# Optimization experiments

Hardware: AMD Instinct MI355X
Metric: run time of the kernel (lower is better)

The kernel has to match this reference:

```python
import jax, jax.numpy as jnp
import numpy as np

LN_EPS = 1e-5
NUM_EXPERTS = 8

def setup_inputs() -> dict:
    key = jax.random.key(0)
    ks = jax.random.split(key, 8)
    B, S, D = 8, 2048, 2048
    R = D // 4  # reduced_dim = 512
    E = NUM_EXPERTS
    scale1 = 1.0 / np.sqrt(D)
    scale2 = 1.0 / np.sqrt(R)
    return {
        "hidden_states": jax.random.normal(ks[0], (B, S, D), dtype=jnp.float32),
        "ln_gamma": jnp.ones((D,), dtype=jnp.float32),
        "ln_beta": jnp.zeros((D,), dtype=jnp.float32),
        "w1": jax.random.uniform(ks[1], (D, R), minval=-scale1, maxval=scale1, dtype=jnp.float32),
        "b1": jax.random.uniform(ks[2], (R,), minval=-scale1, maxval=scale1, dtype=jnp.float32),
        "w2": jax.random.uniform(ks[3], (R, R), minval=-scale2, maxval=scale2, dtype=jnp.float32),
        "b2": jax.random.uniform(ks[4], (R,), minval=-scale2, maxval=scale2, dtype=jnp.float32),
        "wr": jax.random.uniform(ks[5], (R, E), minval=-scale2, maxval=scale2, dtype=jnp.float32),
        "br": jax.random.uniform(ks[6], (E,), minval=-scale2, maxval=scale2, dtype=jnp.float32),
    }

def reference(hidden_states, ln_gamma, ln_beta, w1, b1, w2, b2, wr, br):
    # LayerNorm over last dim (eps matches torch default 1e-5)
    mu = jnp.mean(hidden_states, axis=-1, keepdims=True)
    var = jnp.mean(jnp.square(hidden_states - mu), axis=-1, keepdims=True)
    x = (hidden_states - mu) * jax.lax.rsqrt(var + LN_EPS) * ln_gamma + ln_beta
    # Linear -> GELU (exact, torch default) -> Linear
    h = jax.nn.gelu(jnp.einsum('bsd,dr->bsr', x, w1) + b1, approximate=False)
    t = jnp.einsum('bsr,rq->bsq', h, w2) + b2  # [B,S,R]
    batch_reduced = jnp.sum(t, axis=1)          # [B,R]
    router_logits = batch_reduced @ wr + br     # [B,E]
    # top-1 expert per batch element; one-hot targets via scatter
    expert_indices = jnp.argmax(router_logits, axis=-1)                 # [B]
    targets = jax.nn.one_hot(expert_indices, router_logits.shape[-1],
                             dtype=router_logits.dtype)                 # [B,E]
    # BCE-with-logits, mean over all elements: log(1+e^x) - x*t
    aux_loss = jnp.mean(jnp.logaddexp(0.0, router_logits) - router_logits * targets)
    # mode over batch of top-1 indices (torch .mode returns smallest on ties;
    # argmax of bincount picks the first/smallest max index -> matches)
    counts = jnp.sum(targets, axis=0)
    next_idx = jnp.argmax(counts)
    return aux_loss, next_idx
```

## Files before the change

### kernel.cpp

```cpp
#include <hip/hip_runtime.h>
#include <math.h>

#define D_DIM 2048
#define R_DIM 512
#define E_NUM 8
#define B_NUM 8
#define S_NUM 2048
#define M_DIM 16384
#define LN_EPS 1e-5f

typedef __attribute__((ext_vector_type(8))) short bf16x8;
typedef __attribute__((ext_vector_type(4))) float f32x4;

__device__ __forceinline__ unsigned short f2bf(float f) {
    unsigned u = __float_as_uint(f);
    return (unsigned short)((u + 0x7FFFu + ((u >> 16) & 1u)) >> 16);
}

__device__ __forceinline__ void gload_lds16(const void* g, void* l) {
    __builtin_amdgcn_global_load_lds(
        (const __attribute__((address_space(1))) void*)g,
        (__attribute__((address_space(3))) void*)l, 16, 0, 0);
}

__global__ __launch_bounds__(256) void prep_kernel(float* __restrict__ x,
                                                   const float* __restrict__ gamma,
                                                   const float* __restrict__ beta,
                                                   const float* __restrict__ w1,
                                                   unsigned short* __restrict__ wt,
                                                   float* __restrict__ zbuf) {
    const int t = threadIdx.x;
    if (blockIdx.x < M_DIM) {
        __shared__ float sred[8];
        float* row = x + (size_t)blockIdx.x * D_DIM;
        const float4 v0  = ((const float4*)row)[t];
        const float4 v1  = ((const float4*)row)[t + 256];
        const float4 g0  = ((const float4*)gamma)[t];
        const float4 g1  = ((const float4*)gamma)[t + 256];
        const float4 be0 = ((const float4*)beta)[t];
        const float4 be1 = ((const float4*)beta)[t + 256];

        float s  = v0.x + v0.y + v0.z + v0.w + v1.x + v1.y + v1.z + v1.w;
        float sq = v0.x*v0.x + v0.y*v0.y + v0.z*v0.z + v0.w*v0.w
                 + v1.x*v1.x + v1.y*v1.y + v1.z*v1.z + v1.w*v1.w;
#pragma unroll
        for (int off = 32; off > 0; off >>= 1) {
            s  += __shfl_down(s, off);
            sq += __shfl_down(sq, off);
        }
        if ((t & 63) == 0) { sred[(t >> 6) * 2] = s; sred[(t >> 6) * 2 + 1] = sq; }
        __syncthreads();
        s  = sred[0] + sred[2] + sred[4] + sred[6];
        sq = sred[1] + sred[3] + sred[5] + sred[7];
        const float mu  = s * (1.f / D_DIM);
        const float var = sq * (1.f / D_DIM) - mu * mu;
        const float rs  = rsqrtf(var + LN_EPS);

        ushort4 h0, h1;
        h0.x = f2bf(fmaf((v0.x - mu) * rs, g0.x, be0.x));
        h0.y = f2bf(fmaf((v0.y - mu) * rs, g0.y, be0.y));
        h0.z = f2bf(fmaf((v0.z - mu) * rs, g0.z, be0.z));
        h0.w = f2bf(fmaf((v0.w - mu) * rs, g0.w, be0.w));
        h1.x = f2bf(fmaf((v1.x - mu) * rs, g1.x, be1.x));
        h1.y = f2bf(fmaf((v1.y - mu) * rs, g1.y, be1.y));
        h1.z = f2bf(fmaf((v1.z - mu) * rs, g1.z, be1.z));
        h1.w = f2bf(fmaf((v1.w - mu) * rs, g1.w, be1.w));

        ushort4* rowu = (ushort4*)row;
        rowu[t]       = h0;
        rowu[t + 256] = h1;
    } else if (blockIdx.x < M_DIM + 1024) {
        const int tid = (blockIdx.x - M_DIM) * 256 + t;
        const int n  = tid >> 9;
        const int k4 = tid & 511;
        ushort4 h;
        h.x = f2bf(w1[(size_t)(k4 * 4 + 0) * R_DIM + n]);
        h.y = f2bf(w1[(size_t)(k4 * 4 + 1) * R_DIM + n]);
        h.z = f2bf(w1[(size_t)(k4 * 4 + 2) * R_DIM + n]);
        h.w = f2bf(w1[(size_t)(k4 * 4 + 3) * R_DIM + n]);
        ((ushort4*)wt)[(size_t)n * 512 + k4] = h;
    } else {
        zbuf[(blockIdx.x - M_DIM - 1024) * 256 + t] = 0.f;
    }
}

#define BM 128
#define BN 128
#define BK 64

__global__ __launch_bounds__(256, 2) void gemm_kernel(
    const unsigned short* __restrict__ xs,
    const unsigned short* __restrict__ wt,
    const float* __restrict__ b1,
    float* __restrict__ hsum) {
    __shared__ __align__(16) unsigned short lds[2 * 8192];

    const int t = threadIdx.x, lane = t & 63, wid = t >> 6;
    const int xcd = blockIdx.x & 7, i0 = blockIdx.x >> 3;
    const int n0 = (xcd >> 1) * BN;
    const int m0 = ((xcd & 1) * 64 + i0) * BM;
    const int mw = wid >> 1, nw = wid & 1;
    const int fr = lane & 15, kg = lane >> 4, fr7 = lane & 7;

    f32x4 acc[4][4];
#pragma unroll
    for (int i = 0; i < 4; ++i)
#pragma unroll
        for (int j = 0; j < 4; ++j) acc[i][j] = (f32x4){0.f, 0.f, 0.f, 0.f};

    int srow[4], sgo[4], ldso[4];
#pragma unroll
    for (int ii = 0; ii < 4; ++ii) {
        const int idx = wid * 4 + ii;
        const int o = (idx << 10) + (lane << 4);
        const int r = o >> 7, sl = (o >> 4) & 7;
        srow[ii] = r;
        sgo[ii]  = ((sl ^ (r & 7)) << 4);
        ldso[ii] = (idx << 10);
    }

    int aoff[4], boff[4];
#pragma unroll
    for (int f = 0; f < 4; ++f) {
        aoff[f] = (mw * 64 + f * 16 + fr) * 128;
        boff[f] = (nw * 64 + f * 16 + fr) * 128;
    }
    const char* ldsb = (const char*)lds;

    for (int k0b = 0; k0b < D_DIM * 2; k0b += BK * 2) {
        __syncthreads();
#pragma unroll
        for (int ii = 0; ii < 4; ++ii) {
            const char* a = (const char*)xs + (size_t)(m0 + srow[ii]) * 8192 + k0b + sgo[ii];
            const char* b = (const char*)wt + (size_t)(n0 + srow[ii]) * 4096 + k0b + sgo[ii];
            gload_lds16(a, (char*)lds +     0 + ldso[ii]);
            gload_lds16(b, (char*)lds + 16384 + ldso[ii]);
        }
        __syncthreads();
#pragma unroll
        for (int kk = 0; kk < 2; ++kk) {
            const int sw = ((kk * 4 + kg) ^ fr7) << 4;
            bf16x8 ah[4], bh[4];
#pragma unroll
            for (int f = 0; f < 4; ++f) {
                ah[f] = *(const bf16x8*)(ldsb +     0 + aoff[f] + sw);
                bh[f] = *(const bf16x8*)(ldsb + 16384 + boff[f] + sw);
            }
#pragma unroll
            for (int i = 0; i < 4; ++i)
#pragma unroll
                for (int j = 0; j < 4; ++j)
                    acc[i][j] = __builtin_amdgcn_mfma_f32_16x16x32_bf16(ah[i], bh[j], acc[i][j], 0, 0, 0);
        }
    }

    __syncthreads();
    float* red = (float*)lds;
    float pn[4];
#pragma unroll
    for (int j = 0; j < 4; ++j) pn[j] = 0.f;
#pragma unroll
    for (int j = 0; j < 4; ++j) {
        const float bb = b1[n0 + nw * 64 + j * 16 + fr];
#pragma unroll
        for (int i = 0; i < 4; ++i)
#pragma unroll
            for (int r = 0; r < 4; ++r) {
                const float y = acc[i][j][r] + bb;
                pn[j] += 0.5f * y * (1.f + erff(y * 0.70710678118654752f));
            }
    }
#pragma unroll
    for (int j = 0; j < 4; ++j)
        red[(wid * 4 + kg) * 64 + j * 16 + fr] = pn[j];
    __syncthreads();
    if (t < 128) {
        const int nw2 = t >> 6, cl = t & 63;
        float s2 = 0.f;
#pragma unroll
        for (int mw2 = 0; mw2 < 2; ++mw2)
#pragma unroll
            for (int g = 0; g < 4; ++g)
                s2 += red[((mw2 * 2 + nw2) * 4 + g) * 64 + cl];
        atomicAdd(&hsum[(m0 >> 11) * R_DIM + n0 + t], s2);
    }
}

__global__ void router1_kernel(const float* __restrict__ hsum,
                               const float* __restrict__ w2,
                               const float* __restrict__ b2,
                               float* __restrict__ brd) {
    const int q  = blockIdx.x * 64 + threadIdx.x;
    const int r0 = blockIdx.y * 64;
    float acc[8] = {0, 0, 0, 0, 0, 0, 0, 0};
    for (int r = r0 + threadIdx.y; r < r0 + 64; r += 4) {
        const float w = w2[(size_t)r * R_DIM + q];
#pragma unroll
        for (int b = 0; b < 8; ++b) acc[b] = fmaf(hsum[b * R_DIM + r], w, acc[b]);
    }
    __shared__ float sred[4][8][64];
#pragma unroll
    for (int b = 0; b < 8; ++b) sred[threadIdx.y][b][threadIdx.x] = acc[b];
    __syncthreads();
    if (threadIdx.y == 0) {
        const float bias2 = (blockIdx.y == 0) ? (float)S_NUM * b2[q] : 0.f;
#pragma unroll
        for (int b = 0; b < 8; ++b) {
            float s = sred[0][b][threadIdx.x] + sred[1][b][threadIdx.x]
                    + sred[2][b][threadIdx.x] + sred[3][b][threadIdx.x] + bias2;
            atomicAdd(&brd[b * R_DIM + q], s);
        }
    }
}

__global__ void router2_kernel(const float* __restrict__ brd,
                               const float* __restrict__ wr,
                               const float* __restrict__ br,
                               float* __restrict__ out) {
    __shared__ float part[8][64];
    __shared__ float lg[64];
    const int te = threadIdx.x;
    const int qg = threadIdx.y;
    const int b = te >> 3, e = te & 7;
    float s = 0.f;
    for (int q = qg; q < R_DIM; q += 8)
        s = fmaf(brd[b * R_DIM + q], wr[q * E_NUM + e], s);
    part[qg][te] = s;
    __syncthreads();
    if (qg == 0) {
        float v = br[e];
#pragma unroll
        for (int g = 0; g < 8; ++g) v += part[g][te];
        lg[te] = v;
    }
    __syncthreads();
    if (te == 0 && qg == 0) {
        int cnt[8] = {0, 0, 0, 0, 0, 0, 0, 0};
        float loss = 0.f;
        for (int bb = 0; bb < 8; ++bb) {
            int best = 0;
            float bv = lg[bb * 8];
            for (int ee = 1; ee < 8; ++ee)
                if (lg[bb * 8 + ee] > bv) { bv = lg[bb * 8 + ee]; best = ee; }
            cnt[best]++;
            for (int ee = 0; ee < 8; ++ee) {
                const float xv = lg[bb * 8 + ee];
                loss += fmaxf(xv, 0.f) + log1pf(expf(-fabsf(xv))) - (ee == best ? xv : 0.f);
            }
        }
        out[0] = loss * (1.f / 64.f);
        int ni = 0;
        for (int ee = 1; ee < 8; ++ee)
            if (cnt[ee] > cnt[ni]) ni = ee;
        out[1] = (float)ni;
    }
}

extern "C" void kernel_launch(void* const* d_in, const int* in_sizes, int n_in,
                              void* d_out, int out_size, void* d_ws, size_t ws_size,
                              hipStream_t stream) {
    float* x           = (float*)d_in[0];
    const float* gamma = (const float*)d_in[1];
    const float* beta  = (const float*)d_in[2];
    const float* w1    = (const float*)d_in[3];
    const float* b1    = (const float*)d_in[4];
    const float* w2    = (const float*)d_in[5];
    const float* b2    = (const float*)d_in[6];
    const float* wr    = (const float*)d_in[7];
    const float* br    = (const float*)d_in[8];
    float* out = (float*)d_out;
    float* ws  = (float*)d_ws;

    float* hsum = ws;
    float* brd  = ws + 4096;
    unsigned short* wt = (unsigned short*)(ws + 8192);

    prep_kernel<<<dim3(M_DIM + 1024 + 32), dim3(256), 0, stream>>>(
        x, gamma, beta, w1, wt, ws);
    gemm_kernel<<<dim3(512), dim3(256), 0, stream>>>(
        (const unsigned short*)x, wt, b1, hsum);
    router1_kernel<<<dim3(8, 8), dim3(64, 4), 0, stream>>>(hsum, w2, b2, brd);
    router2_kernel<<<dim3(1), dim3(64, 8), 0, stream>>>(brd, wr, br, out);
}
```

Before: 307.9 us.

## Double-buffer GEMM LDS tiles and fuse router kernels into one block

The GEMM main loop now uses two LDS buffers, issuing global-to-LDS loads for the next K tile while MFMAs run on the current one, and drops one barrier per iteration. This doubles LDS use to 64KB per block, which may cut occupancy below the two blocks per CU that launch_bounds asks for. The two router kernels are merged into a single 512-thread block that stages hsum in LDS and computes the w2 projection, logits and loss directly. That removes one launch and the brd atomics and zeroing, but the w2 step now runs on a single workgroup.

```diff
diff --git a/kernel.cpp b/kernel.cpp
--- a/kernel.cpp
+++ b/kernel.cpp
@@ -93,7 +93,7 @@
     const unsigned short* __restrict__ wt,
     const float* __restrict__ b1,
     float* __restrict__ hsum) {
-    __shared__ __align__(16) unsigned short lds[2 * 8192];
+    __shared__ __align__(16) unsigned short lds[2 * 16384];
 
     const int t = threadIdx.x, lane = t & 63, wid = t >> 6;
     const int xcd = blockIdx.x & 7, i0 = blockIdx.x >> 3;
@@ -125,26 +125,34 @@
         aoff[f] = (mw * 64 + f * 16 + fr) * 128;
         boff[f] = (nw * 64 + f * 16 + fr) * 128;
     }
-    const char* ldsb = (const char*)lds;
-
-    for (int k0b = 0; k0b < D_DIM * 2; k0b += BK * 2) {
-        __syncthreads();
+    const char* xb = (const char*)xs;
+    const char* wb = (const char*)wt;
+
+    auto stage = [&](int bsel, int k0b) {
+        char* base = (char*)lds + bsel * 32768;
 #pragma unroll
         for (int ii = 0; ii < 4; ++ii) {
-            const char* a = (const char*)xs + (size_t)(m0 + srow[ii]) * 8192 + k0b + sgo[ii];
-            const char* b = (const char*)wt + (size_t)(n0 + srow[ii]) * 4096 + k0b + sgo[ii];
-            gload_lds16(a, (char*)lds +     0 + ldso[ii]);
-            gload_lds16(b, (char*)lds + 16384 + ldso[ii]);
-        }
-        __syncthreads();
+            const char* a = xb + (size_t)(m0 + srow[ii]) * 8192 + k0b + sgo[ii];
+            const char* b = wb + (size_t)(n0 + srow[ii]) * 4096 + k0b + sgo[ii];
+            gload_lds16(a, base +     0 + ldso[ii]);
+            gload_lds16(b, base + 16384 + ldso[ii]);
+        }
+    };
+
+    stage(0, 0);
+    __syncthreads();
+    int buf = 0;
+    for (int it = 0; it < 32; ++it) {
+        if (it < 31) stage(buf ^ 1, (it + 1) << 7);
+        const char* ab = (const char*)lds + buf * 32768;
 #pragma unroll
         for (int kk = 0; kk < 2; ++kk) {
             const int sw = ((kk * 4 + kg) ^ fr7) << 4;
             bf16x8 ah[4], bh[4];
 #pragma unroll
             for (int f = 0; f < 4; ++f) {
-                ah[f] = *(const bf16x8*)(ldsb +     0 + aoff[f] + sw);
-                bh[f] = *(const bf16x8*)(ldsb + 16384 + boff[f] + sw);
+                ah[f] = *(const bf16x8*)(ab +     0 + aoff[f] + sw);
+                bh[f] = *(const bf16x8*)(ab + 16384 + boff[f] + sw);
             }
 #pragma unroll
             for (int i = 0; i < 4; ++i)
@@ -152,9 +160,10 @@
                 for (int j = 0; j < 4; ++j)
                     acc[i][j] = __builtin_amdgcn_mfma_f32_16x16x32_bf16(ah[i], bh[j], acc[i][j], 0, 0, 0);
         }
-    }
-
-    __syncthreads();
+        __syncthreads();
+        buf ^= 1;
+    }
+
     float* red = (float*)lds;
     float pn[4];
 #pragma unroll
@@ -186,41 +195,33 @@
     }
 }
 
-__global__ void router1_kernel(const float* __restrict__ hsum,
-                               const float* __restrict__ w2,
-                               const float* __restrict__ b2,
-                               float* __restrict__ brd) {
-    const int q  = blockIdx.x * 64 + threadIdx.x;
-    const int r0 = blockIdx.y * 64;
-    float acc[8] = {0, 0, 0, 0, 0, 0, 0, 0};
-    for (int r = r0 + threadIdx.y; r < r0 + 64; r += 4) {
-        const float w = w2[(size_t)r * R_DIM + q];
-#pragma unroll
-        for (int b = 0; b < 8; ++b) acc[b] = fmaf(hsum[b * R_DIM + r], w, acc[b]);
-    }
-    __shared__ float sred[4][8][64];
-#pragma unroll
-    for (int b = 0; b < 8; ++b) sred[threadIdx.y][b][threadIdx.x] = acc[b];
-    __syncthreads();
-    if (threadIdx.y == 0) {
-        const float bias2 = (blockIdx.y == 0) ? (float)S_NUM * b2[q] : 0.f;
-#pragma unroll
-        for (int b = 0; b < 8; ++b) {
-            float s = sred[0][b][threadIdx.x] + sred[1][b][threadIdx.x]
-                    + sred[2][b][threadIdx.x] + sred[3][b][threadIdx.x] + bias2;
-            atomicAdd(&brd[b * R_DIM + q], s);
-        }
-    }
-}
-
-__global__ void router2_kernel(const float* __restrict__ brd,
-                               const float* __restrict__ wr,
-                               const float* __restrict__ br,
-                               float* __restrict__ out) {
+__global__ __launch_bounds__(512) void router_kernel(const float* __restrict__ hsum,
+                                                     const float* __restrict__ w2,
+                                                     const float* __restrict__ b2,
+                                                     const float* __restrict__ wr,
+                                                     const float* __restrict__ br,
+                                                     float* __restrict__ out) {
+    __shared__ float hs[B_NUM * R_DIM];
+    __shared__ float brd[B_NUM * R_DIM];
     __shared__ float part[8][64];
     __shared__ float lg[64];
-    const int te = threadIdx.x;
-    const int qg = threadIdx.y;
+    const int t = threadIdx.x;
+    for (int i = t; i < B_NUM * R_DIM; i += 512) hs[i] = hsum[i];
+    __syncthreads();
+
+    float acc[B_NUM] = {0, 0, 0, 0, 0, 0, 0, 0};
+#pragma unroll 4
+    for (int r = 0; r < R_DIM; ++r) {
+        const float w = w2[(size_t)r * R_DIM + t];
+#pragma unroll
+        for (int b = 0; b < B_NUM; ++b) acc[b] = fmaf(hs[b * R_DIM + r], w, acc[b]);
+    }
+    const float bias2 = (float)S_NUM * b2[t];
+#pragma unroll
+    for (int b = 0; b < B_NUM; ++b) brd[b * R_DIM + t] = acc[b] + bias2;
+    __syncthreads();
+
+    const int te = t & 63, qg = t >> 6;
     const int b = te >> 3, e = te & 7;
     float s = 0.f;
     for (int q = qg; q < R_DIM; q += 8)
@@ -234,7 +235,7 @@
         lg[te] = v;
     }
     __syncthreads();
-    if (te == 0 && qg == 0) {
+    if (t == 0) {
         int cnt[8] = {0, 0, 0, 0, 0, 0, 0, 0};
         float loss = 0.f;
         for (int bb = 0; bb < 8; ++bb) {
@@ -272,13 +273,11 @@
     float* ws  = (float*)d_ws;
 
     float* hsum = ws;
-    float* brd  = ws + 4096;
-    unsigned short* wt = (unsigned short*)(ws + 8192);
-
-    prep_kernel<<<dim3(M_DIM + 1024 + 32), dim3(256), 0, stream>>>(
-        x, gamma, beta, w1, wt, ws);
+    unsigned short* wt = (unsigned short*)(ws + 4096);
+
+    prep_kernel<<<dim3(M_DIM + 1024 + 16), dim3(256), 0, stream>>>(
+        x, gamma, beta, w1, wt, hsum);
     gemm_kernel<<<dim3(512), dim3(256), 0, stream>>>(
         (const unsigned short*)x, wt, b1, hsum);
-    router1_kernel<<<dim3(8, 8), dim3(64, 4), 0, stream>>>(hsum, w2, b2, brd);
-    router2_kernel<<<dim3(1), dim3(64, 8), 0, stream>>>(brd, wr, br, out);
-}
+    router_kernel<<<dim3(1), dim3(512), 0, stream>>>(hsum, w2, b2, wr, br, out);
+}
```

Measured after the change: 362.2 us. 1.18x slower.
